# Performance work log

Hardware: AMD Instinct MI355X
Metric: run time of the kernel (lower is better)

## Reference

```python
import jax, jax.numpy as jnp
import numpy as np

CONTACT_THRESH = 0.01
COLLISION_THRESH = 0.005
WEIGHT_PEN = 100.0
WEIGHT_MISS = 10.0
# MANO fingertip + palm contact-zone vertex indices (hardcoded in module)
CONTACT_IDX = np.array([745, 317, 444, 556, 673, 95, 182, 234, 279, 320])

SCALE = 0.1  # place points in a 0.1 m cube so mm-scale thresholds are meaningful


def setup_inputs() -> dict:
    key = jax.random.key(0)
    k1, k2, k3, k4 = jax.random.split(key, 4)
    B, NH, V = 8, 778, 40000
    hand_verts = jax.random.uniform(k1, (B, NH, 3), dtype=jnp.float32) * SCALE
    obj_verts = jax.random.uniform(k2, (B, V, 3), dtype=jnp.float32) * SCALE
    hand_faces = jax.random.randint(k3, (1538, 3), 0, NH, dtype=jnp.int64 if jax.config.read('jax_enable_x64') else jnp.int32)
    obj_faces = jax.random.randint(k4, (79996, 3), 0, V, dtype=jnp.int64 if jax.config.read('jax_enable_x64') else jnp.int32)
    return {"hand_verts": hand_verts, "obj_verts": obj_verts,
            "hand_faces": hand_faces, "obj_faces": obj_faces}


def _min_dists(a, b):
    """Brute-force 1-NN: min Euclidean distance from each point in a [B,N,3] to b [B,M,3] -> [B,N]."""
    a_sq = jnp.sum(a * a, axis=-1, keepdims=True)          # [B,N,1]
    b_sq = jnp.sum(b * b, axis=-1)                          # [B,M]
    ab = jnp.einsum('bnd,bmd->bnm', a, b)                   # [B,N,M]
    d2 = jnp.maximum(a_sq + b_sq[:, None, :] - 2.0 * ab, 0.0)
    return jnp.sqrt(jnp.min(d2, axis=2))                    # [B,N]


def _masked_mean(vals, mask):
    cnt = jnp.sum(mask)
    s = jnp.sum(jnp.where(mask, vals, 0.0))
    return jnp.where(cnt > 0, s / jnp.maximum(cnt, 1).astype(vals.dtype), jnp.zeros((), vals.dtype))


def reference(hand_verts, obj_verts, hand_faces, obj_faces):
    # faces are unused by the loss (as in the torch module)
    idx = jnp.asarray(CONTACT_IDX)
    # distances are computed under no_grad / detached in the original
    dists = jax.lax.stop_gradient(_min_dists(hand_verts, obj_verts))              # [B,778]
    contact_dists = jax.lax.stop_gradient(_min_dists(hand_verts[:, idx, :], obj_verts))  # [B,10]

    pen_mask = dists < COLLISION_THRESH
    pen_loss = _masked_mean((COLLISION_THRESH - dists) ** 2, pen_mask)

    att_mask = (contact_dists > COLLISION_THRESH) & (contact_dists < CONTACT_THRESH)
    att_loss = _masked_mean(contact_dists ** 2, att_mask)

    contact_loss = WEIGHT_PEN * pen_loss + WEIGHT_MISS * att_loss
    dist_mean = jnp.mean(dists)
    num_contacts = jnp.sum(att_mask).astype(jnp.int32)
    num_penetrations = jnp.sum(pen_mask).astype(jnp.int32)
    return (contact_loss, pen_loss, att_loss, dist_mean, num_contacts, num_penetrations)
```

## Files before the change

### kernel.cpp

```cpp
#include <hip/hip_runtime.h>
#include <math.h>

constexpr int NH    = 778;
constexpr int GRIDC = 16;
constexpr int NCELL = GRIDC * GRIDC * GRIDC;
constexpr int CAP   = 40;
constexpr float CELL     = 0.1f / GRIDC;
constexpr float INV_CELL = GRIDC / 0.1f;

__device__ __forceinline__ int clampc(int v) {
    return min(GRIDC - 1, max(0, v));
}

__global__ __launch_bounds__(256) void bin_kernel(
    const float* __restrict__ obj,
    int* __restrict__ cnt,
    int* __restrict__ ocnt,
    float4* __restrict__ buckets,
    float4* __restrict__ ovf,
    int total, int V)
{
    const int i = blockIdx.x * 256 + threadIdx.x;
    if (i >= total) return;
    const float x = obj[3 * i + 0];
    const float y = obj[3 * i + 1];
    const float z = obj[3 * i + 2];
    const int cx = clampc((int)(x * INV_CELL));
    const int cy = clampc((int)(y * INV_CELL));
    const int cz = clampc((int)(z * INV_CELL));
    const int b = i / V;
    const int cell = b * NCELL + (cz * GRIDC + cy) * GRIDC + cx;
    const int idx = atomicAdd(&cnt[cell], 1);
    if (idx < CAP) {
        buckets[(size_t)cell * CAP + idx] = make_float4(x, y, z, 0.f);
    } else {
        const int oi = atomicAdd(ocnt, 1);
        ovf[oi] = make_float4(x, y, z, __int_as_float(b));
    }
}

__global__ __launch_bounds__(256) void query_kernel(
    const float* __restrict__ hand,
    const int* __restrict__ cnt,
    const float4* __restrict__ buckets,
    const float4* __restrict__ ovf,
    const int* __restrict__ ocnt,
    float* __restrict__ dist,
    int B)
{
    const int gid  = blockIdx.x * 256 + threadIdx.x;
    const int i    = gid >> 6;
    const int lane = gid & 63;
    if (i >= B * NH) return;
    const int b = i / NH;

    const float hx = hand[3 * i + 0];
    const float hy = hand[3 * i + 1];
    const float hz = hand[3 * i + 2];
    const int hcx = clampc((int)(hx * INV_CELL));
    const int hcy = clampc((int)(hy * INV_CELL));
    const int hcz = clampc((int)(hz * INV_CELL));
    const int cbase = b * NCELL;

    float best = 3.4e38f;

    if (lane < 54) {
        const int cl  = lane >> 1;
        const int sub = lane & 1;
        const int cx = hcx + (cl % 3) - 1;
        const int cy = hcy + ((cl / 3) % 3) - 1;
        const int cz = hcz + (cl / 9) - 1;
        if (cx >= 0 && cx < GRIDC && cy >= 0 && cy < GRIDC &&
            cz >= 0 && cz < GRIDC) {
            const int cell = cbase + (cz * GRIDC + cy) * GRIDC + cx;
            const int n = min(cnt[cell], CAP);
            const float4* bp = buckets + (size_t)cell * CAP;
            for (int k = sub; k < n; k += 2) {
                const float4 p = bp[k];
                const float dx = p.x - hx, dy = p.y - hy, dz = p.z - hz;
                best = fminf(best, fmaf(dx, dx, fmaf(dy, dy, dz * dz)));
            }
        }
    }

    const int on = *ocnt;
    for (int k = lane; k < on; k += 64) {
        const float4 p = ovf[k];
        if (__float_as_int(p.w) == b) {
            const float dx = p.x - hx, dy = p.y - hy, dz = p.z - hz;
            best = fminf(best, fmaf(dx, dx, fmaf(dy, dy, dz * dz)));
        }
    }

#pragma unroll
    for (int d = 1; d < 64; d <<= 1) best = fminf(best, __shfl_xor(best, d));

    for (int r = 2; r < GRIDC; ++r) {
        const float bnd = (float)(r - 1) * CELL;
        if (best <= bnd * bnd) break;
        const int side = 2 * r + 1;
        const int ncells = side * side * side;
        for (int ci = lane; ci < ncells; ci += 64) {
            const int dx = ci % side - r;
            const int dy = (ci / side) % side - r;
            const int dz = ci / (side * side) - r;
            if (max(max(abs(dx), abs(dy)), abs(dz)) != r) continue;
            const int cx = hcx + dx, cy = hcy + dy, cz = hcz + dz;
            if (cx < 0 || cx >= GRIDC || cy < 0 || cy >= GRIDC ||
                cz < 0 || cz >= GRIDC) continue;
            const int cell = cbase + (cz * GRIDC + cy) * GRIDC + cx;
            const int n = min(cnt[cell], CAP);
            const float4* bp = buckets + (size_t)cell * CAP;
            for (int k = 0; k < n; ++k) {
                const float4 p = bp[k];
                const float ddx = p.x - hx, ddy = p.y - hy, ddz = p.z - hz;
                best = fminf(best, fmaf(ddx, ddx, fmaf(ddy, ddy, ddz * ddz)));
            }
        }
#pragma unroll
        for (int d = 1; d < 64; d <<= 1) best = fminf(best, __shfl_xor(best, d));
    }

    if (lane == 0) dist[i] = best;
}

typedef float v2f __attribute__((ext_vector_type(2)));
constexpr int FT = 16, FG = 4, FBLK = 256, FCHUNK = 2560;
constexpr int FNBX = (NH + FG * FT - 1) / (FG * FT);
constexpr int FLPP = FCHUNK / FBLK, FPP = FLPP / 2;

__global__ __launch_bounds__(FBLK, 2) void nn_brute_kernel(
    const float* __restrict__ hand, const float* __restrict__ obj,
    unsigned int* __restrict__ minb, int V)
{
    __shared__ float s_red[4][16 * 65];
    const int bx = blockIdx.x, c = blockIdx.y, b = blockIdx.z;
    const int tid = threadIdx.x, wave = tid >> 6, lane = tid & 63;
    const int r = lane & 15, seg = lane >> 4;
    const float* ob = obj + (size_t)b * V * 3;
    const int base = c * FCHUNK + tid;
    v2f ox2[FPP], oy2[FPP], oz2[FPP], oq2[FPP];
#pragma unroll
    for (int p = 0; p < FPP; ++p) {
        const int ja = min(base + (2 * p + 0) * FBLK, V - 1);
        const int jb = min(base + (2 * p + 1) * FBLK, V - 1);
        const float xa = ob[3 * ja], ya = ob[3 * ja + 1], za = ob[3 * ja + 2];
        const float xb = ob[3 * jb], yb = ob[3 * jb + 1], zb = ob[3 * jb + 2];
        ox2[p] = (v2f){-2.f * xa, -2.f * xb};
        oy2[p] = (v2f){-2.f * ya, -2.f * yb};
        oz2[p] = (v2f){-2.f * za, -2.f * zb};
        oq2[p] = (v2f){fmaf(xa, xa, fmaf(ya, ya, za * za)),
                       fmaf(xb, xb, fmaf(yb, yb, zb * zb))};
    }
    const float* hb = hand + (size_t)b * NH * 3;
    float* sw = &s_red[wave][0];
#pragma unroll 1
    for (int g = 0; g < FG; ++g) {
        float hx[FT], hy[FT], hz[FT], m[FT];
#pragma unroll
        for (int t = 0; t < FT; ++t) {
            const int h = min((bx * FG + g) * FT + t, NH - 1);
            hx[t] = hb[3 * h]; hy[t] = hb[3 * h + 1]; hz[t] = hb[3 * h + 2];
            m[t] = 3.4e38f;
        }
#pragma unroll
        for (int p = 0; p < FPP; ++p) {
#pragma unroll
            for (int t = 0; t < FT; ++t) {
                v2f a = __builtin_elementwise_fma(ox2[p], (v2f){hx[t], hx[t]}, oq2[p]);
                a = __builtin_elementwise_fma(oy2[p], (v2f){hy[t], hy[t]}, a);
                a = __builtin_elementwise_fma(oz2[p], (v2f){hz[t], hz[t]}, a);
                m[t] = fminf(fminf(a.x, a.y), m[t]);
            }
        }
#pragma unroll
        for (int t = 0; t < FT; ++t) {
            const float hq = fmaf(hx[t], hx[t], fmaf(hy[t], hy[t], hz[t] * hz[t]));
            sw[t * 65 + lane] = m[t] + hq;
        }
        __builtin_amdgcn_wave_barrier();
        float v = 3.4e38f;
        const int rb = r * 65 + seg * 16;
#pragma unroll
        for (int j = 0; j < 16; ++j) v = fminf(v, sw[rb + j]);
        __builtin_amdgcn_wave_barrier();
        v = fminf(v, __shfl_xor(v, 16));
        v = fminf(v, __shfl_xor(v, 32));
        if (seg == 0) {
            const int hidx = (bx * FG + g) * FT + r;
            if (hidx < NH) {
                const unsigned bits = __float_as_uint(fmaxf(v, 0.f));
                unsigned int* p = &minb[b * NH + hidx];
                if (bits < *((volatile unsigned int*)p)) atomicMin(p, bits);
            }
        }
    }
}

__global__ __launch_bounds__(256) void finalize_kernel(
    const float* __restrict__ dist, float* __restrict__ out, int B)
{
    constexpr float COLL = 0.005f;
    constexpr float CONT = 0.01f;
    const int total = B * NH;
    const int tid = threadIdx.x;

    double sum_d = 0.0, pen_sum = 0.0, att_sum = 0.0;
    int pen_cnt = 0, att_cnt = 0;
    for (int i = tid; i < total; i += 256) {
        const float d = sqrtf(fmaxf(dist[i], 0.f));
        sum_d += (double)d;
        if (d < COLL) { const float t = COLL - d; pen_sum += (double)(t * t); pen_cnt++; }
        const int n = i % NH;
        const bool isc = (n == 745) | (n == 317) | (n == 444) | (n == 556) |
                         (n == 673) | (n == 95)  | (n == 182) | (n == 234) |
                         (n == 279) | (n == 320);
        if (isc & (d > COLL) & (d < CONT)) { att_sum += (double)(d * d); att_cnt++; }
    }

    __shared__ double sd[256], sp[256], sa[256];
    __shared__ int    cp[256], ca[256];
    sd[tid] = sum_d; sp[tid] = pen_sum; sa[tid] = att_sum;
    cp[tid] = pen_cnt; ca[tid] = att_cnt;
    __syncthreads();
    for (int off = 128; off > 0; off >>= 1) {
        if (tid < off) {
            sd[tid] += sd[tid + off]; sp[tid] += sp[tid + off];
            sa[tid] += sa[tid + off];
            cp[tid] += cp[tid + off]; ca[tid] += ca[tid + off];
        }
        __syncthreads();
    }
    if (tid == 0) {
        const double pen_loss = cp[0] > 0 ? sp[0] / (double)cp[0] : 0.0;
        const double att_loss = ca[0] > 0 ? sa[0] / (double)ca[0] : 0.0;
        out[0] = (float)(100.0 * pen_loss + 10.0 * att_loss);
        out[1] = (float)pen_loss;
        out[2] = (float)att_loss;
        out[3] = (float)(sd[0] / (double)total);
        out[4] = (float)ca[0];
        out[5] = (float)cp[0];
    }
}

extern "C" void kernel_launch(void* const* d_in, const int* in_sizes, int n_in,
                              void* d_out, int out_size, void* d_ws, size_t ws_size,
                              hipStream_t stream) {
    const float* hand = (const float*)d_in[0];
    const float* obj  = (const float*)d_in[1];

    const int B = in_sizes[0] / (NH * 3);
    const int V = in_sizes[1] / (B * 3);
    const int total = B * V;

    float* dist = (float*)d_ws;
    char* base = (char*)d_ws;
    size_t off = 65536;
    int* cnt = (int*)(base + off);
    const size_t cnt_bytes = (size_t)B * NCELL * sizeof(int);
    int* ocnt = (int*)(base + off + cnt_bytes);
    size_t boff = (off + cnt_bytes + 256) & ~(size_t)255;
    float4* buckets = (float4*)(base + boff);
    const size_t bkt_bytes = (size_t)B * NCELL * CAP * sizeof(float4);
    float4* ovf = (float4*)(base + boff + bkt_bytes);
    const size_t need = boff + bkt_bytes + (size_t)total * sizeof(float4);

    if (ws_size >= need) {
        hipMemsetAsync(cnt, 0, cnt_bytes + 64, stream);
        bin_kernel<<<(total + 255) / 256, 256, 0, stream>>>(
            obj, cnt, ocnt, buckets, ovf, total, V);
        const int qthreads = B * NH * 64;
        query_kernel<<<(qthreads + 255) / 256, 256, 0, stream>>>(
            hand, cnt, buckets, ovf, ocnt, dist, B);
    } else {
        hipMemsetAsync(d_ws, 0x7F, (size_t)B * NH * sizeof(unsigned int), stream);
        dim3 grid(FNBX, (V + FCHUNK - 1) / FCHUNK, B);
        nn_brute_kernel<<<grid, FBLK, 0, stream>>>(hand, obj,
                                                   (unsigned int*)d_ws, V);
    }
    finalize_kernel<<<1, 256, 0, stream>>>(dist, (float*)d_out, B);
}
```

Baseline: 100.3 us.

## Fuse loss reduction into grid query kernel and pad cell counters

Folds the finalize step into the spatial-grid query kernel. Each block reduces its per-vertex loss terms in shared memory, adds them into 32 sharded global double accumulators with atomics, and the last block (found through a ticket counter) computes the final outputs. This removes one kernel launch and the single-block finalize pass. Cell counters are also padded to a 16-int stride to cut atomic contention on shared cache lines during binning, at the cost of a larger memset.

```diff
diff --git a/kernel.cpp b/kernel.cpp
--- a/kernel.cpp
+++ b/kernel.cpp
@@ -5,8 +5,10 @@
 constexpr int GRIDC = 16;
 constexpr int NCELL = GRIDC * GRIDC * GRIDC;
 constexpr int CAP   = 40;
+constexpr int CS    = 16;
 constexpr float CELL     = 0.1f / GRIDC;
 constexpr float INV_CELL = GRIDC / 0.1f;
+constexpr int NSH = 32;
 
 __device__ __forceinline__ int clampc(int v) {
     return min(GRIDC - 1, max(0, v));
@@ -30,7 +32,7 @@
     const int cz = clampc((int)(z * INV_CELL));
     const int b = i / V;
     const int cell = b * NCELL + (cz * GRIDC + cy) * GRIDC + cx;
-    const int idx = atomicAdd(&cnt[cell], 1);
+    const int idx = atomicAdd(&cnt[(size_t)cell * CS], 1);
     if (idx < CAP) {
         buckets[(size_t)cell * CAP + idx] = make_float4(x, y, z, 0.f);
     } else {
@@ -39,89 +41,150 @@
     }
 }
 
-__global__ __launch_bounds__(256) void query_kernel(
+__global__ __launch_bounds__(256) void query_fused_kernel(
     const float* __restrict__ hand,
     const int* __restrict__ cnt,
     const float4* __restrict__ buckets,
     const float4* __restrict__ ovf,
     const int* __restrict__ ocnt,
-    float* __restrict__ dist,
-    int B)
+    double* __restrict__ shd,
+    int* __restrict__ shi,
+    int* __restrict__ ticket,
+    float* __restrict__ out,
+    int nq, int B)
 {
-    const int gid  = blockIdx.x * 256 + threadIdx.x;
-    const int i    = gid >> 6;
-    const int lane = gid & 63;
-    if (i >= B * NH) return;
-    const int b = i / NH;
-
-    const float hx = hand[3 * i + 0];
-    const float hy = hand[3 * i + 1];
-    const float hz = hand[3 * i + 2];
-    const int hcx = clampc((int)(hx * INV_CELL));
-    const int hcy = clampc((int)(hy * INV_CELL));
-    const int hcz = clampc((int)(hz * INV_CELL));
-    const int cbase = b * NCELL;
+    constexpr float COLL = 0.005f;
+    constexpr float CONT = 0.01f;
+    const int tid  = threadIdx.x;
+    const int wave = tid >> 6;
+    const int lane = tid & 63;
+    const int i    = blockIdx.x * 4 + wave;
+    const bool valid = i < nq;
 
     float best = 3.4e38f;
 
-    if (lane < 54) {
-        const int cl  = lane >> 1;
-        const int sub = lane & 1;
-        const int cx = hcx + (cl % 3) - 1;
-        const int cy = hcy + ((cl / 3) % 3) - 1;
-        const int cz = hcz + (cl / 9) - 1;
-        if (cx >= 0 && cx < GRIDC && cy >= 0 && cy < GRIDC &&
-            cz >= 0 && cz < GRIDC) {
-            const int cell = cbase + (cz * GRIDC + cy) * GRIDC + cx;
-            const int n = min(cnt[cell], CAP);
-            const float4* bp = buckets + (size_t)cell * CAP;
-            for (int k = sub; k < n; k += 2) {
-                const float4 p = bp[k];
+    if (valid) {
+        const int b = i / NH;
+        const float hx = hand[3 * i + 0];
+        const float hy = hand[3 * i + 1];
+        const float hz = hand[3 * i + 2];
+        const int hcx = clampc((int)(hx * INV_CELL));
+        const int hcy = clampc((int)(hy * INV_CELL));
+        const int hcz = clampc((int)(hz * INV_CELL));
+        const int cbase = b * NCELL;
+
+        if (lane < 54) {
+            const int cl  = lane >> 1;
+            const int sub = lane & 1;
+            const int cx = hcx + (cl % 3) - 1;
+            const int cy = hcy + ((cl / 3) % 3) - 1;
+            const int cz = hcz + (cl / 9) - 1;
+            if (cx >= 0 && cx < GRIDC && cy >= 0 && cy < GRIDC &&
+                cz >= 0 && cz < GRIDC) {
+                const int cell = cbase + (cz * GRIDC + cy) * GRIDC + cx;
+                const int n = min(cnt[(size_t)cell * CS], CAP);
+                const float4* bp = buckets + (size_t)cell * CAP;
+                for (int k = sub; k < n; k += 2) {
+                    const float4 p = bp[k];
+                    const float dx = p.x - hx, dy = p.y - hy, dz = p.z - hz;
+                    best = fminf(best, fmaf(dx, dx, fmaf(dy, dy, dz * dz)));
+                }
+            }
+        }
+
+        const int on = *ocnt;
+        for (int k = lane; k < on; k += 64) {
+            const float4 p = ovf[k];
+            if (__float_as_int(p.w) == b) {
                 const float dx = p.x - hx, dy = p.y - hy, dz = p.z - hz;
                 best = fminf(best, fmaf(dx, dx, fmaf(dy, dy, dz * dz)));
             }
         }
-    }
-
-    const int on = *ocnt;
-    for (int k = lane; k < on; k += 64) {
-        const float4 p = ovf[k];
-        if (__float_as_int(p.w) == b) {
-            const float dx = p.x - hx, dy = p.y - hy, dz = p.z - hz;
-            best = fminf(best, fmaf(dx, dx, fmaf(dy, dy, dz * dz)));
-        }
-    }
-
-#pragma unroll
-    for (int d = 1; d < 64; d <<= 1) best = fminf(best, __shfl_xor(best, d));
-
-    for (int r = 2; r < GRIDC; ++r) {
-        const float bnd = (float)(r - 1) * CELL;
-        if (best <= bnd * bnd) break;
-        const int side = 2 * r + 1;
-        const int ncells = side * side * side;
-        for (int ci = lane; ci < ncells; ci += 64) {
-            const int dx = ci % side - r;
-            const int dy = (ci / side) % side - r;
-            const int dz = ci / (side * side) - r;
-            if (max(max(abs(dx), abs(dy)), abs(dz)) != r) continue;
-            const int cx = hcx + dx, cy = hcy + dy, cz = hcz + dz;
-            if (cx < 0 || cx >= GRIDC || cy < 0 || cy >= GRIDC ||
-                cz < 0 || cz >= GRIDC) continue;
-            const int cell = cbase + (cz * GRIDC + cy) * GRIDC + cx;
-            const int n = min(cnt[cell], CAP);
-            const float4* bp = buckets + (size_t)cell * CAP;
-            for (int k = 0; k < n; ++k) {
-                const float4 p = bp[k];
-                const float ddx = p.x - hx, ddy = p.y - hy, ddz = p.z - hz;
-                best = fminf(best, fmaf(ddx, ddx, fmaf(ddy, ddy, ddz * ddz)));
-            }
-        }
+
 #pragma unroll
         for (int d = 1; d < 64; d <<= 1) best = fminf(best, __shfl_xor(best, d));
-    }
-
-    if (lane == 0) dist[i] = best;
+
+        for (int r = 2; r < GRIDC; ++r) {
+            const float bnd = (float)(r - 1) * CELL;
+            if (best <= bnd * bnd) break;
+            const int side = 2 * r + 1;
+            const int ncells = side * side * side;
+            for (int ci = lane; ci < ncells; ci += 64) {
+                const int dx = ci % side - r;
+                const int dy = (ci / side) % side - r;
+                const int dz = ci / (side * side) - r;
+                if (max(max(abs(dx), abs(dy)), abs(dz)) != r) continue;
+                const int cx = hcx + dx, cy = hcy + dy, cz = hcz + dz;
+                if (cx < 0 || cx >= GRIDC || cy < 0 || cy >= GRIDC ||
+                    cz < 0 || cz >= GRIDC) continue;
+                const int cell = cbase + (cz * GRIDC + cy) * GRIDC + cx;
+                const int n = min(cnt[(size_t)cell * CS], CAP);
+                const float4* bp = buckets + (size_t)cell * CAP;
+                for (int k = 0; k < n; ++k) {
+                    const float4 p = bp[k];
+                    const float ddx = p.x - hx, ddy = p.y - hy, ddz = p.z - hz;
+                    best = fminf(best, fmaf(ddx, ddx, fmaf(ddy, ddy, ddz * ddz)));
+                }
+            }
+#pragma unroll
+            for (int d = 1; d < 64; d <<= 1) best = fminf(best, __shfl_xor(best, d));
+        }
+    }
+
+    __shared__ double ssd[4], ssp[4], ssa[4];
+    __shared__ int scp[4], sca[4];
+    if (lane == 0) {
+        double sd = 0.0, sp = 0.0, sa = 0.0;
+        int cp = 0, ca = 0;
+        if (valid) {
+            const float d = sqrtf(fmaxf(best, 0.f));
+            sd = (double)d;
+            if (d < COLL) { const float t = COLL - d; sp = (double)(t * t); cp = 1; }
+            const int n = i % NH;
+            const bool isc = (n == 745) | (n == 317) | (n == 444) | (n == 556) |
+                             (n == 673) | (n == 95)  | (n == 182) | (n == 234) |
+                             (n == 279) | (n == 320);
+            if (isc & (d > COLL) & (d < CONT)) { sa = (double)(d * d); ca = 1; }
+        }
+        ssd[wave] = sd; ssp[wave] = sp; ssa[wave] = sa;
+        scp[wave] = cp; sca[wave] = ca;
+    }
+    __syncthreads();
+    if (tid == 0) {
+        const double sd = ssd[0] + ssd[1] + ssd[2] + ssd[3];
+        const double sp = ssp[0] + ssp[1] + ssp[2] + ssp[3];
+        const double sa = ssa[0] + ssa[1] + ssa[2] + ssa[3];
+        const int cp = scp[0] + scp[1] + scp[2] + scp[3];
+        const int ca = sca[0] + sca[1] + sca[2] + sca[3];
+        const int sh = (int)(blockIdx.x & (NSH - 1));
+        atomicAdd(&shd[sh * 3 + 0], sd);
+        atomicAdd(&shd[sh * 3 + 1], sp);
+        atomicAdd(&shd[sh * 3 + 2], sa);
+        atomicAdd(&shi[sh * 2 + 0], cp);
+        atomicAdd(&shi[sh * 2 + 1], ca);
+        __threadfence();
+        const int t = atomicAdd(ticket, 1);
+        if (t == (int)gridDim.x - 1) {
+            __threadfence();
+            double fsd = 0.0, fsp = 0.0, fsa = 0.0;
+            int fcp = 0, fca = 0;
+            for (int s = 0; s < NSH; ++s) {
+                fsd += __hip_atomic_load(&shd[s * 3 + 0], __ATOMIC_RELAXED, __HIP_MEMORY_SCOPE_AGENT);
+                fsp += __hip_atomic_load(&shd[s * 3 + 1], __ATOMIC_RELAXED, __HIP_MEMORY_SCOPE_AGENT);
+                fsa += __hip_atomic_load(&shd[s * 3 + 2], __ATOMIC_RELAXED, __HIP_MEMORY_SCOPE_AGENT);
+                fcp += __hip_atomic_load(&shi[s * 2 + 0], __ATOMIC_RELAXED, __HIP_MEMORY_SCOPE_AGENT);
+                fca += __hip_atomic_load(&shi[s * 2 + 1], __ATOMIC_RELAXED, __HIP_MEMORY_SCOPE_AGENT);
+            }
+            const double pen_loss = fcp > 0 ? fsp / (double)fcp : 0.0;
+            const double att_loss = fca > 0 ? fsa / (double)fca : 0.0;
+            out[0] = (float)(100.0 * pen_loss + 10.0 * att_loss);
+            out[1] = (float)pen_loss;
+            out[2] = (float)att_loss;
+            out[3] = (float)(fsd / (double)nq);
+            out[4] = (float)fca;
+            out[5] = (float)fcp;
+        }
+    }
 }
 
 typedef float v2f __attribute__((ext_vector_type(2)));
@@ -252,31 +315,34 @@
     const int B = in_sizes[0] / (NH * 3);
     const int V = in_sizes[1] / (B * 3);
     const int total = B * V;
-
-    float* dist = (float*)d_ws;
+    const int nq = B * NH;
+
     char* base = (char*)d_ws;
     size_t off = 65536;
-    int* cnt = (int*)(base + off);
-    const size_t cnt_bytes = (size_t)B * NCELL * sizeof(int);
-    int* ocnt = (int*)(base + off + cnt_bytes);
-    size_t boff = (off + cnt_bytes + 256) & ~(size_t)255;
+    int*    ticket = (int*)(base + off);
+    int*    ocnt   = (int*)(base + off + 4);
+    double* shd    = (double*)(base + off + 64);
+    int*    shi    = (int*)(base + off + 64 + NSH * 3 * 8);
+    int*    cnt    = (int*)(base + off + 4096);
+    const size_t cnt_bytes = (size_t)B * NCELL * CS * sizeof(int);
+    const size_t boff = (off + 4096 + cnt_bytes + 255) & ~(size_t)255;
     float4* buckets = (float4*)(base + boff);
     const size_t bkt_bytes = (size_t)B * NCELL * CAP * sizeof(float4);
     float4* ovf = (float4*)(base + boff + bkt_bytes);
     const size_t need = boff + bkt_bytes + (size_t)total * sizeof(float4);
 
     if (ws_size >= need) {
-        hipMemsetAsync(cnt, 0, cnt_bytes + 64, stream);
+        hipMemsetAsync(base + off, 0, 4096 + cnt_bytes, stream);
         bin_kernel<<<(total + 255) / 256, 256, 0, stream>>>(
             obj, cnt, ocnt, buckets, ovf, total, V);
-        const int qthreads = B * NH * 64;
-        query_kernel<<<(qthreads + 255) / 256, 256, 0, stream>>>(
-            hand, cnt, buckets, ovf, ocnt, dist, B);
+        const int qblocks = (nq * 64 + 255) / 256;
+        query_fused_kernel<<<qblocks, 256, 0, stream>>>(
+            hand, cnt, buckets, ovf, ocnt, shd, shi, ticket, (float*)d_out, nq, B);
     } else {
-        hipMemsetAsync(d_ws, 0x7F, (size_t)B * NH * sizeof(unsigned int), stream);
+        hipMemsetAsync(d_ws, 0x7F, (size_t)nq * sizeof(unsigned int), stream);
         dim3 grid(FNBX, (V + FCHUNK - 1) / FCHUNK, B);
         nn_brute_kernel<<<grid, FBLK, 0, stream>>>(hand, obj,
                                                    (unsigned int*)d_ws, V);
-    }
-    finalize_kernel<<<1, 256, 0, stream>>>(dist, (float*)d_out, B);
-}
+        finalize_kernel<<<1, 256, 0, stream>>>((const float*)d_ws, (float*)d_out, B);
+    }
+}
```

After: 130.0 us. 1.3x slower.
